# Kernel tuning notes

Hardware: AMD Instinct MI355X
Metric: run time of the kernel (lower is better)

Reference implementation:

```python
import jax, jax.numpy as jnp
import numpy as np

G, N_PER_G, S, DEG, EMB, LAYERS = 64, 64, 8, 4, 128, 5


def _build_structure():
    """Ring graphs (degree DEG) with per-root windows of S nodes.
    Returns all integer index arrays for the tuple-sparse conv."""
    N = G * N_PER_G
    P = N * S          # (i, j) pairs
    T = P * S          # (i, j, k) tuples, k fastest
    deltas = np.array([1, 2, -1, -2])
    roots = np.arange(N)
    gbase = (roots // N_PER_G) * N_PER_G
    # window(i): S consecutive nodes in the same graph
    win = ((roots % N_PER_G)[:, None] + np.arange(S)) % N_PER_G + gbase[:, None]  # [N,S]
    tupleid0 = np.repeat(roots, S * S)
    tupleid1 = np.repeat(win.ravel(), S)
    # valid (k-offset, delta) combos so that l = k + delta stays inside window
    ok_g, di_g = np.meshgrid(np.arange(S), np.arange(DEG), indexing='ij')
    ol = ok_g + deltas[di_g]
    m = (ol >= 0) & (ol < S)
    ok_v, di_v, ol_v = ok_g[m], di_g[m], ol[m]        # [26]
    pairs = np.arange(P)
    msg_dst = (pairs[:, None] * S + ok_v[None, :]).ravel()
    msg_src = (pairs[:, None] * S + ol_v[None, :]).ravel()
    i_of_pair = pairs // S
    k_glob = ((i_of_pair % N_PER_G)[:, None] + ok_v[None, :]) % N_PER_G \
             + ((i_of_pair // N_PER_G) * N_PER_G)[:, None]
    msg_edge = (k_glob * DEG + di_v[None, :]).ravel()  # edge id = u*DEG + delta_idx
    seg_pair = np.arange(T) // S   # tuple -> (i,j) pair
    seg_node = np.arange(P) // S   # pair  -> root node i
    batch = np.repeat(np.arange(G), N_PER_G)
    return N, P, T, tupleid0, tupleid1, msg_src, msg_dst, msg_edge, seg_pair, seg_node, batch


def setup_inputs() -> dict:
    rng = np.random.default_rng(0)
    N, P, T, t0, t1, ms, md, me, sp, sn, batch = _build_structure()
    E = N * DEG
    i32 = lambda a: jnp.asarray(a, jnp.int32)
    key = jax.random.key(0)
    ks = jax.random.split(key, 8)
    sc = 0.05
    inp = {
        'x': i32(rng.integers(0, 32, N)),
        'edge_attr': i32(rng.integers(0, 16, E)),
        'tuplefeat': i32(rng.integers(0, 16, (T, 2))),
        'batch': i32(batch),
        'tupleid0': i32(t0), 'tupleid1': i32(t1),
        'msg_src': i32(ms), 'msg_dst': i32(md), 'msg_edge': i32(me),
        'seg_pair': i32(sp), 'seg_node': i32(sn),
        'num_graphs': G,
        'emb_x': jax.random.normal(ks[0], (32, EMB), jnp.float32) * sc,
        'emb_ea': jax.random.normal(ks[1], (16, EMB), jnp.float32) * sc,
        'emb_tf': jax.random.normal(ks[2], (16, EMB // 2), jnp.float32) * sc,
        'w_ti': jax.random.normal(ks[3], (EMB, EMB), jnp.float32) * sc,
        'b_ti': jnp.zeros((EMB,), jnp.float32),
        'w_conv': jax.random.normal(ks[4], (LAYERS, EMB, EMB), jnp.float32) * sc,
        'b_conv': jnp.zeros((LAYERS, EMB), jnp.float32),
        'w_pred': jax.random.normal(ks[5], (EMB, 1), jnp.float32) * sc,
        'b_pred': jnp.zeros((1,), jnp.float32),
    }
    return inp


def reference(x, edge_attr, tuplefeat, batch, tupleid0, tupleid1,
              msg_src, msg_dst, msg_edge, seg_pair, seg_node, num_graphs,
              emb_x, emb_ea, emb_tf, w_ti, b_ti, w_conv, b_conv, w_pred, b_pred):
    T = tuplefeat.shape[0]
    N = x.shape[0]
    P = seg_node.shape[0]
    # InputEncoder
    xe = emb_x[x]                                   # [N, E]
    ea = emb_ea[edge_attr]                          # [E_edges, E]
    tf = emb_tf[tuplefeat].reshape(T, -1)           # [T, 2, E/2] -> [T, E]
    # tupleinit: x[t0] * lin(x)[t1] * tuplefeat
    Xv = xe[tupleid0] * (xe @ w_ti + b_ti)[tupleid1] * tf   # [T, E]

    def layer(carry, wb):
        w, b = wb
        msgs = carry[msg_src] * ea[msg_edge]                         # [M, E]
        agg = jax.ops.segment_sum(msgs, msg_dst, num_segments=T)      # [T, E]
        return carry + jax.nn.relu(agg @ w + b), None                 # residual

    Xv, _ = jax.lax.scan(layer, Xv, (w_conv, b_conv))
    # pooling2tuple (max over k), pooling2nodes (sum over j), npool (sum over batch)
    pair = jax.ops.segment_max(Xv, seg_pair, num_segments=P)          # [P, E]
    node = jax.ops.segment_sum(pair, seg_node, num_segments=N)        # [N, E]
    graph = jax.ops.segment_sum(node, batch, num_segments=num_graphs) # [G, E]
    return graph @ w_pred + b_pred                                    # [G, 1]
```

## Files before the change

### kernel.cpp

```cpp
#include <hip/hip_runtime.h>
#include <hip/hip_bf16.h>

#define EMB 128

typedef __attribute__((ext_vector_type(8))) short short8;
typedef __attribute__((ext_vector_type(4))) float floatx4;

static constexpr int OKv[26] = {0,0,1,1,1,2,2,2,2,3,3,3,3,4,4,4,4,5,5,5,5,6,6,6,7,7};
static constexpr int DIv[26] = {0,1,0,1,2,0,1,2,3,0,1,2,3,0,1,2,3,0,1,2,3,0,2,3,2,3};
static constexpr int OLv[26] = {1,2,2,3,0,3,4,1,0,4,5,2,1,5,6,3,2,6,7,4,3,7,5,4,6,5};

__device__ __forceinline__ float2 ld2(const float* p) { return *(const float2*)p; }

__device__ __forceinline__ unsigned bf16_rne_hi(float x) {
  unsigned u = __float_as_uint(x);
  return (u + 0x7FFFu + ((u >> 16) & 1u)) & 0xFFFF0000u;
}
__device__ __forceinline__ float bf16hi_f(float x) {
  return __uint_as_float(bf16_rne_hi(x));
}
__device__ __forceinline__ unsigned cvt_pk_bf16(float a, float b) {
  __hip_bfloat162 h = __float22bfloat162_rn(make_float2(a, b));
  unsigned r; __builtin_memcpy(&r, &h, 4); return r;
}

union FragU { unsigned u[4]; uint4 q; short8 v; };


__global__ __launch_bounds__(512) void prep_kernel(
    const float* __restrict__ emb_x,
    const float* __restrict__ w_ti,
    const float* __restrict__ b_ti,
    const float* __restrict__ w_conv,
    const float* __restrict__ b_pred,
    float* __restrict__ lin32,
    uint4* __restrict__ wfrag,
    float* __restrict__ out) {
  const int b = blockIdx.x, tid = threadIdx.x;
  if (b < 32) {
    __shared__ float red[4][EMB];
    const int e = tid & 127, fh = tid >> 7;
    const float* xr = emb_x + b * EMB;
    float s = 0.f;
    #pragma unroll 8
    for (int f = fh * 32; f < fh * 32 + 32; ++f)
      s = fmaf(xr[f], w_ti[f * EMB + e], s);
    red[fh][e] = s;
    __syncthreads();
    if (fh == 0)
      lin32[b * EMB + e] =
          b_ti[e] + ((red[0][e] + red[1][e]) + (red[2][e] + red[3][e]));
  } else if (b < 72) {
    const int id   = (b - 32) * 512 + tid;
    const int lane = id & 63;
    const int f    = id >> 6;
    const int pass = f & 1;
    const int u    = (f >> 1) & 7;
    const int t    = (f >> 4) & 3;
    const int l    = f >> 6;
    const int q    = lane >> 4, n = lane & 15;
    const int cN   = 2 * ((u >> 1) * 16 + n) + (u & 1);
    unsigned w[4] = {0u, 0u, 0u, 0u};
    #pragma unroll
    for (int j = 0; j < 8; ++j) {
      const int kk = t * 32 + q * 8 + j;
      float val = w_conv[l * (EMB * EMB) + kk * EMB + cN];
      if (pass) val = val - bf16hi_f(val);
      const unsigned bb = bf16_rne_hi(val);
      w[j >> 1] |= (j & 1) ? bb : (bb >> 16);
    }
    wfrag[id] = make_uint4(w[0], w[1], w[2], w[3]);
  } else {
    if (tid < 64) out[tid] = b_pred[0];
  }
}

__global__ __launch_bounds__(256)
void i2gnn_mfma(
    const int* __restrict__ x,
    const int* __restrict__ edge_attr,
    const int* __restrict__ tuplefeat,
    const float* __restrict__ emb_x,
    const float* __restrict__ emb_tf,
    const float* __restrict__ emb_ea,
    const float* __restrict__ lin32,
    const float* __restrict__ b_conv,
    const float* __restrict__ w_pred,
    const uint4* __restrict__ wfrag,
    float* __restrict__ out)
{
  __shared__ __align__(16) unsigned fragA[2 * 64 * 68];

  const int tid = threadIdx.x;
  const int wv = tid >> 6, lane = tid & 63;
  const int m16 = lane & 15, q2 = lane >> 4;
  const int pc = wv * 16 + m16;
  const int c0 = pc * 2;

  const int i = blockIdx.x;
  const int ibase = i & ~63, io = i & 63;
  const int g = i >> 6;

  unsigned pk[4] = {0u, 0u, 0u, 0u};
  #pragma unroll
  for (int m = 0; m < 26; ++m) {
    const int kg = ibase + ((io + OKv[m]) & 63);
    const unsigned a = (unsigned)edge_attr[(kg << 2) + DIv[m]];
    pk[m >> 3] |= a << ((m & 7) * 4);
  }

  const int xi = x[i];
  const float2 xe = ld2(emb_x + xi * EMB + c0);
  float2 lj[2];
  #pragma unroll
  for (int ps = 0; ps < 2; ++ps) {
    const int jn = ibase + ((io + 2 * q2 + ps) & 63);
    lj[ps] = ld2(lin32 + x[jn] * EMB + c0);
  }
  floatx4 X[2][4];
  #pragma unroll
  for (int mt = 0; mt < 4; ++mt) {
    const int ps = mt & 1, kb = (mt >> 1) * 4;
    const int t0 = (i * 8 + 2 * q2 + ps) << 3;
    #pragma unroll
    for (int r = 0; r < 4; ++r) {
      const int2 tf2 = *(const int2*)(tuplefeat + 2 * (t0 + kb + r));
      const int row = (c0 < 64) ? tf2.x : tf2.y;
      const float2 tf = ld2(emb_tf + row * 64 + (c0 & 63));
      X[0][mt][r] = xe.x * lj[ps].x * tf.x;
      X[1][mt][r] = xe.y * lj[ps].y * tf.y;
    }
  }

  for (int l = 0; l < 5; ++l) {
    float acc[2][2][8];
    #pragma unroll
    for (int v = 0; v < 2; ++v)
      #pragma unroll
      for (int ps = 0; ps < 2; ++ps)
        #pragma unroll
        for (int k = 0; k < 8; ++k) acc[v][ps][k] = 0.f;
    #pragma unroll
    for (int m = 0; m < 26; ++m) {
      const unsigned attr = (pk[m >> 3] >> ((m & 7) * 4)) & 15u;
      const float2 e = ld2(emb_ea + attr * EMB + c0);
      const int ok = OKv[m], ol = OLv[m];
      const int mtb = 2 * (ol >> 2), rl = ol & 3;
      acc[0][0][ok] = fmaf(X[0][mtb + 0][rl], e.x, acc[0][0][ok]);
      acc[0][1][ok] = fmaf(X[0][mtb + 1][rl], e.x, acc[0][1][ok]);
      acc[1][0][ok] = fmaf(X[1][mtb + 0][rl], e.y, acc[1][0][ok]);
      acc[1][1][ok] = fmaf(X[1][mtb + 1][rl], e.y, acc[1][1][ok]);
    }
    #pragma unroll
    for (int ps = 0; ps < 2; ++ps)
      #pragma unroll
      for (int k = 0; k < 8; ++k) {
        const float a0 = acc[0][ps][k], a1 = acc[1][ps][k];
        const unsigned hi = cvt_pk_bf16(a0, a1);
        const float r0 = a0 - __uint_as_float(hi << 16);
        const float r1 = a1 - __uint_as_float(hi & 0xFFFF0000u);
        const int row = (ps + 2 * (k >> 2)) * 16 + q2 * 4 + (k & 3);
        fragA[row * 68 + pc] = hi;
        fragA[4352 + row * 68 + pc] = cvt_pk_bf16(r0, r1);
      }
    __syncthreads();

    floatx4 C[2][4];
    #pragma unroll
    for (int v = 0; v < 2; ++v)
      #pragma unroll
      for (int mt = 0; mt < 4; ++mt) C[v][mt] = (floatx4){0.f, 0.f, 0.f, 0.f};

    #pragma unroll
    for (int kt = 0; kt < 4; ++kt) {
      const uint4* wp0 = wfrag + ((((l * 4 + kt) * 8 + 2 * wv) * 2) << 6);
      FragU B0h, B0l, B1h, B1l;
      B0h.q = wp0[lane];        B0l.q = wp0[64 + lane];
      B1h.q = wp0[128 + lane];  B1l.q = wp0[192 + lane];
      #pragma unroll
      for (int mt = 0; mt < 4; ++mt) {
        const unsigned* fa = fragA + (mt * 16 + m16) * 68 + kt * 16 + q2 * 4;
        FragU Ah, Al;
        Ah.q = *(const uint4*)fa;
        Al.q = *(const uint4*)(fa + 4352);
        C[0][mt] = __builtin_amdgcn_mfma_f32_16x16x32_bf16(Ah.v, B0h.v, C[0][mt], 0, 0, 0);
        C[0][mt] = __builtin_amdgcn_mfma_f32_16x16x32_bf16(Al.v, B0h.v, C[0][mt], 0, 0, 0);
        C[0][mt] = __builtin_amdgcn_mfma_f32_16x16x32_bf16(Ah.v, B0l.v, C[0][mt], 0, 0, 0);
        C[1][mt] = __builtin_amdgcn_mfma_f32_16x16x32_bf16(Ah.v, B1h.v, C[1][mt], 0, 0, 0);
        C[1][mt] = __builtin_amdgcn_mfma_f32_16x16x32_bf16(Al.v, B1h.v, C[1][mt], 0, 0, 0);
        C[1][mt] = __builtin_amdgcn_mfma_f32_16x16x32_bf16(Ah.v, B1l.v, C[1][mt], 0, 0, 0);
      }
    }
    __syncthreads();

    const float2 bc = ld2(b_conv + l * EMB + c0);
    #pragma unroll
    for (int mt = 0; mt < 4; ++mt)
      #pragma unroll
      for (int r = 0; r < 4; ++r) {
        X[0][mt][r] += fmaxf(C[0][mt][r] + bc.x, 0.f);
        X[1][mt][r] += fmaxf(C[1][mt][r] + bc.y, 0.f);
      }
  }

  const float2 wp = ld2(w_pred + c0);
  float s = 0.f;
  #pragma unroll
  for (int v = 0; v < 2; ++v) {
    float p0 = -3.4e38f, p1 = -3.4e38f;
    #pragma unroll
    for (int r = 0; r < 4; ++r) {
      p0 = fmaxf(p0, fmaxf(X[v][0][r], X[v][2][r]));
      p1 = fmaxf(p1, fmaxf(X[v][1][r], X[v][3][r]));
    }
    s = fmaf(p0 + p1, v ? wp.y : wp.x, s);
  }
  #pragma unroll
  for (int off = 32; off; off >>= 1) s += __shfl_xor(s, off, 64);
  if (lane == 0) atomicAdd(out + g, s);
}

extern "C" void kernel_launch(void* const* d_in, const int* in_sizes, int n_in,
                              void* d_out, int out_size, void* d_ws, size_t ws_size,
                              hipStream_t stream) {
  const int*   x         = (const int*)d_in[0];
  const int*   edge_attr = (const int*)d_in[1];
  const int*   tuplefeat = (const int*)d_in[2];
  const float* emb_x     = (const float*)d_in[12];
  const float* emb_ea    = (const float*)d_in[13];
  const float* emb_tf    = (const float*)d_in[14];
  const float* w_ti      = (const float*)d_in[15];
  const float* b_ti      = (const float*)d_in[16];
  const float* w_conv    = (const float*)d_in[17];
  const float* b_conv    = (const float*)d_in[18];
  const float* w_pred    = (const float*)d_in[19];
  const float* b_pred    = (const float*)d_in[20];
  float* out = (float*)d_out;
  float* lin32 = (float*)d_ws;
  uint4* wfrag = (uint4*)((char*)d_ws + 32 * EMB * 4);

  hipLaunchKernelGGL(prep_kernel, dim3(73), dim3(512), 0, stream,
                     emb_x, w_ti, b_ti, w_conv, b_pred, lin32, wfrag, out);
  hipLaunchKernelGGL(i2gnn_mfma, dim3(4096), dim3(256), 0, stream,
                     x, edge_attr, tuplefeat, emb_x, emb_tf, emb_ea, lin32,
                     b_conv, w_pred, wfrag, out);
}
```

Baseline: 301.0 us.

## Split each root into two 128-thread blocks with 4-channel-per-thread float4 layout

Each root node's work now goes to two blocks of two waves, each handling four j-pairs, where before one four-wave block handled all eight. Each lane now owns four contiguous channels loaded with float4. The weight fragment column mapping and the LDS fragment layout are changed to match, and each wave issues MFMAs for four N-tiles by two M-tiles. The aim is wider vector loads, smaller blocks for more scheduling flexibility, and more B-fragment reuse per loaded A fragment. In exchange, the per-root edge-attribute packing and embedding loads are now repeated across twice as many blocks, and each thread holds more registers.

```diff
diff --git a/kernel.cpp b/kernel.cpp
--- a/kernel.cpp
+++ b/kernel.cpp
@@ -10,7 +10,7 @@
 static constexpr int DIv[26] = {0,1,0,1,2,0,1,2,3,0,1,2,3,0,1,2,3,0,1,2,3,0,2,3,2,3};
 static constexpr int OLv[26] = {1,2,2,3,0,3,4,1,0,4,5,2,1,5,6,3,2,6,7,4,3,7,5,4,6,5};
 
-__device__ __forceinline__ float2 ld2(const float* p) { return *(const float2*)p; }
+__device__ __forceinline__ float4 ld4(const float* p) { return *(const float4*)p; }
 
 __device__ __forceinline__ unsigned bf16_rne_hi(float x) {
   unsigned u = __float_as_uint(x);
@@ -59,7 +59,7 @@
     const int t    = (f >> 4) & 3;
     const int l    = f >> 6;
     const int q    = lane >> 4, n = lane & 15;
-    const int cN   = 2 * ((u >> 1) * 16 + n) + (u & 1);
+    const int cN   = (u >> 2) * 64 + n * 4 + (u & 3);
     unsigned w[4] = {0u, 0u, 0u, 0u};
     #pragma unroll
     for (int j = 0; j < 8; ++j) {
@@ -75,7 +75,7 @@
   }
 }
 
-__global__ __launch_bounds__(256)
+__global__ __launch_bounds__(128)
 void i2gnn_mfma(
     const int* __restrict__ x,
     const int* __restrict__ edge_attr,
@@ -89,15 +89,16 @@
     const uint4* __restrict__ wfrag,
     float* __restrict__ out)
 {
-  __shared__ __align__(16) unsigned fragA[2 * 64 * 68];
+  __shared__ __align__(16) unsigned fragA[2 * 32 * 68];
 
   const int tid = threadIdx.x;
   const int wv = tid >> 6, lane = tid & 63;
   const int m16 = lane & 15, q2 = lane >> 4;
-  const int pc = wv * 16 + m16;
-  const int c0 = pc * 2;
-
-  const int i = blockIdx.x;
+  const int c0 = (wv * 16 + m16) * 4;
+
+  const int b = blockIdx.x;
+  const int i = b >> 1;
+  const int half = b & 1;
   const int ibase = i & ~63, io = i & 63;
   const int g = i >> 6;
 
@@ -109,112 +110,104 @@
     pk[m >> 3] |= a << ((m & 7) * 4);
   }
 
-  const int xi = x[i];
-  const float2 xe = ld2(emb_x + xi * EMB + c0);
-  float2 lj[2];
-  #pragma unroll
-  for (int ps = 0; ps < 2; ++ps) {
-    const int jn = ibase + ((io + 2 * q2 + ps) & 63);
-    lj[ps] = ld2(lin32 + x[jn] * EMB + c0);
-  }
-  floatx4 X[2][4];
-  #pragma unroll
-  for (int mt = 0; mt < 4; ++mt) {
-    const int ps = mt & 1, kb = (mt >> 1) * 4;
-    const int t0 = (i * 8 + 2 * q2 + ps) << 3;
-    #pragma unroll
-    for (int r = 0; r < 4; ++r) {
-      const int2 tf2 = *(const int2*)(tuplefeat + 2 * (t0 + kb + r));
-      const int row = (c0 < 64) ? tf2.x : tf2.y;
-      const float2 tf = ld2(emb_tf + row * 64 + (c0 & 63));
-      X[0][mt][r] = xe.x * lj[ps].x * tf.x;
-      X[1][mt][r] = xe.y * lj[ps].y * tf.y;
-    }
+  const int jj = half * 4 + q2;
+  const int jn = ibase + ((io + jj) & 63);
+  const float4 xe = ld4(emb_x + x[i] * EMB + c0);
+  const float4 lj = ld4(lin32 + x[jn] * EMB + c0);
+  float4 X[8];
+  const int t0 = (i * 8 + jj) * 8;
+  #pragma unroll
+  for (int k = 0; k < 8; ++k) {
+    const int2 tf2 = *(const int2*)(tuplefeat + 2 * (t0 + k));
+    const int row = (c0 < 64) ? tf2.x : tf2.y;
+    const float4 tf = ld4(emb_tf + row * 64 + (c0 & 63));
+    X[k] = make_float4(xe.x * lj.x * tf.x, xe.y * lj.y * tf.y,
+                       xe.z * lj.z * tf.z, xe.w * lj.w * tf.w);
   }
 
   for (int l = 0; l < 5; ++l) {
-    float acc[2][2][8];
-    #pragma unroll
-    for (int v = 0; v < 2; ++v)
-      #pragma unroll
-      for (int ps = 0; ps < 2; ++ps)
-        #pragma unroll
-        for (int k = 0; k < 8; ++k) acc[v][ps][k] = 0.f;
+    float4 acc[8];
+    #pragma unroll
+    for (int k = 0; k < 8; ++k) acc[k] = make_float4(0.f, 0.f, 0.f, 0.f);
     #pragma unroll
     for (int m = 0; m < 26; ++m) {
       const unsigned attr = (pk[m >> 3] >> ((m & 7) * 4)) & 15u;
-      const float2 e = ld2(emb_ea + attr * EMB + c0);
+      const float4 e = ld4(emb_ea + attr * EMB + c0);
       const int ok = OKv[m], ol = OLv[m];
-      const int mtb = 2 * (ol >> 2), rl = ol & 3;
-      acc[0][0][ok] = fmaf(X[0][mtb + 0][rl], e.x, acc[0][0][ok]);
-      acc[0][1][ok] = fmaf(X[0][mtb + 1][rl], e.x, acc[0][1][ok]);
-      acc[1][0][ok] = fmaf(X[1][mtb + 0][rl], e.y, acc[1][0][ok]);
-      acc[1][1][ok] = fmaf(X[1][mtb + 1][rl], e.y, acc[1][1][ok]);
-    }
-    #pragma unroll
-    for (int ps = 0; ps < 2; ++ps)
-      #pragma unroll
-      for (int k = 0; k < 8; ++k) {
-        const float a0 = acc[0][ps][k], a1 = acc[1][ps][k];
-        const unsigned hi = cvt_pk_bf16(a0, a1);
-        const float r0 = a0 - __uint_as_float(hi << 16);
-        const float r1 = a1 - __uint_as_float(hi & 0xFFFF0000u);
-        const int row = (ps + 2 * (k >> 2)) * 16 + q2 * 4 + (k & 3);
-        fragA[row * 68 + pc] = hi;
-        fragA[4352 + row * 68 + pc] = cvt_pk_bf16(r0, r1);
+      acc[ok].x = fmaf(X[ol].x, e.x, acc[ok].x);
+      acc[ok].y = fmaf(X[ol].y, e.y, acc[ok].y);
+      acc[ok].z = fmaf(X[ol].z, e.z, acc[ok].z);
+      acc[ok].w = fmaf(X[ol].w, e.w, acc[ok].w);
+    }
+    #pragma unroll
+    for (int k = 0; k < 8; ++k) {
+      const unsigned h0 = cvt_pk_bf16(acc[k].x, acc[k].y);
+      const unsigned h1 = cvt_pk_bf16(acc[k].z, acc[k].w);
+      const float r0 = acc[k].x - __uint_as_float(h0 << 16);
+      const float r1 = acc[k].y - __uint_as_float(h0 & 0xFFFF0000u);
+      const float r2 = acc[k].z - __uint_as_float(h1 << 16);
+      const float r3 = acc[k].w - __uint_as_float(h1 & 0xFFFF0000u);
+      const int off = ((k >> 2) * 16 + q2 * 4 + (k & 3)) * 68 + (wv * 16 + m16) * 2;
+      *(uint2*)(fragA + off) = make_uint2(h0, h1);
+      *(uint2*)(fragA + 2176 + off) = make_uint2(cvt_pk_bf16(r0, r1),
+                                                 cvt_pk_bf16(r2, r3));
+    }
+    __syncthreads();
+
+    floatx4 C[4][2];
+    #pragma unroll
+    for (int ul = 0; ul < 4; ++ul)
+      #pragma unroll
+      for (int mt = 0; mt < 2; ++mt) C[ul][mt] = (floatx4){0.f, 0.f, 0.f, 0.f};
+
+    #pragma unroll
+    for (int kt = 0; kt < 4; ++kt) {
+      const uint4* wp0 = wfrag + ((((l * 4 + kt) * 8 + wv * 4) * 2) << 6);
+      FragU Bh[4], Bl[4];
+      #pragma unroll
+      for (int ul = 0; ul < 4; ++ul) {
+        Bh[ul].q = wp0[ul * 128 + lane];
+        Bl[ul].q = wp0[ul * 128 + 64 + lane];
       }
-    __syncthreads();
-
-    floatx4 C[2][4];
-    #pragma unroll
-    for (int v = 0; v < 2; ++v)
-      #pragma unroll
-      for (int mt = 0; mt < 4; ++mt) C[v][mt] = (floatx4){0.f, 0.f, 0.f, 0.f};
-
-    #pragma unroll
-    for (int kt = 0; kt < 4; ++kt) {
-      const uint4* wp0 = wfrag + ((((l * 4 + kt) * 8 + 2 * wv) * 2) << 6);
-      FragU B0h, B0l, B1h, B1l;
-      B0h.q = wp0[lane];        B0l.q = wp0[64 + lane];
-      B1h.q = wp0[128 + lane];  B1l.q = wp0[192 + lane];
-      #pragma unroll
-      for (int mt = 0; mt < 4; ++mt) {
+      #pragma unroll
+      for (int mt = 0; mt < 2; ++mt) {
         const unsigned* fa = fragA + (mt * 16 + m16) * 68 + kt * 16 + q2 * 4;
         FragU Ah, Al;
         Ah.q = *(const uint4*)fa;
-        Al.q = *(const uint4*)(fa + 4352);
-        C[0][mt] = __builtin_amdgcn_mfma_f32_16x16x32_bf16(Ah.v, B0h.v, C[0][mt], 0, 0, 0);
-        C[0][mt] = __builtin_amdgcn_mfma_f32_16x16x32_bf16(Al.v, B0h.v, C[0][mt], 0, 0, 0);
-        C[0][mt] = __builtin_amdgcn_mfma_f32_16x16x32_bf16(Ah.v, B0l.v, C[0][mt], 0, 0, 0);
-        C[1][mt] = __builtin_amdgcn_mfma_f32_16x16x32_bf16(Ah.v, B1h.v, C[1][mt], 0, 0, 0);
-        C[1][mt] = __builtin_amdgcn_mfma_f32_16x16x32_bf16(Al.v, B1h.v, C[1][mt], 0, 0, 0);
-        C[1][mt] = __builtin_amdgcn_mfma_f32_16x16x32_bf16(Ah.v, B1l.v, C[1][mt], 0, 0, 0);
+        Al.q = *(const uint4*)(fa + 2176);
+        #pragma unroll
+        for (int ul = 0; ul < 4; ++ul) {
+          C[ul][mt] = __builtin_amdgcn_mfma_f32_16x16x32_bf16(Ah.v, Bh[ul].v, C[ul][mt], 0, 0, 0);
+          C[ul][mt] = __builtin_amdgcn_mfma_f32_16x16x32_bf16(Al.v, Bh[ul].v, C[ul][mt], 0, 0, 0);
+          C[ul][mt] = __builtin_amdgcn_mfma_f32_16x16x32_bf16(Ah.v, Bl[ul].v, C[ul][mt], 0, 0, 0);
+        }
       }
     }
     __syncthreads();
 
-    const float2 bc = ld2(b_conv + l * EMB + c0);
-    #pragma unroll
-    for (int mt = 0; mt < 4; ++mt)
+    const float4 bc = ld4(b_conv + l * EMB + c0);
+    #pragma unroll
+    for (int mt = 0; mt < 2; ++mt)
       #pragma unroll
       for (int r = 0; r < 4; ++r) {
-        X[0][mt][r] += fmaxf(C[0][mt][r] + bc.x, 0.f);
-        X[1][mt][r] += fmaxf(C[1][mt][r] + bc.y, 0.f);
+        const int k = mt * 4 + r;
+        X[k].x += fmaxf(C[0][mt][r] + bc.x, 0.f);
+        X[k].y += fmaxf(C[1][mt][r] + bc.y, 0.f);
+        X[k].z += fmaxf(C[2][mt][r] + bc.z, 0.f);
+        X[k].w += fmaxf(C[3][mt][r] + bc.w, 0.f);
       }
   }
 
-  const float2 wp = ld2(w_pred + c0);
-  float s = 0.f;
-  #pragma unroll
-  for (int v = 0; v < 2; ++v) {
-    float p0 = -3.4e38f, p1 = -3.4e38f;
-    #pragma unroll
-    for (int r = 0; r < 4; ++r) {
-      p0 = fmaxf(p0, fmaxf(X[v][0][r], X[v][2][r]));
-      p1 = fmaxf(p1, fmaxf(X[v][1][r], X[v][3][r]));
-    }
-    s = fmaf(p0 + p1, v ? wp.y : wp.x, s);
-  }
+  float4 pv = X[0];
+  #pragma unroll
+  for (int k = 1; k < 8; ++k) {
+    pv.x = fmaxf(pv.x, X[k].x);
+    pv.y = fmaxf(pv.y, X[k].y);
+    pv.z = fmaxf(pv.z, X[k].z);
+    pv.w = fmaxf(pv.w, X[k].w);
+  }
+  const float4 wp = ld4(w_pred + c0);
+  float s = pv.x * wp.x + pv.y * wp.y + pv.z * wp.z + pv.w * wp.w;
   #pragma unroll
   for (int off = 32; off; off >>= 1) s += __shfl_xor(s, off, 64);
   if (lane == 0) atomicAdd(out + g, s);
@@ -241,7 +234,7 @@
 
   hipLaunchKernelGGL(prep_kernel, dim3(73), dim3(512), 0, stream,
                      emb_x, w_ti, b_ti, w_conv, b_pred, lin32, wfrag, out);
-  hipLaunchKernelGGL(i2gnn_mfma, dim3(4096), dim3(256), 0, stream,
+  hipLaunchKernelGGL(i2gnn_mfma, dim3(8192), dim3(128), 0, stream,
                      x, edge_attr, tuplefeat, emb_x, emb_tf, emb_ea, lin32,
                      b_conv, w_pred, wfrag, out);
 }
```

Measured after the change: 308.6 us. 2.5% more time.
